# Performance work log

Measured on AMD Instinct MI355X. Metric: run time of the kernel, lower is better.

Reference implementation:

```python
import jax, jax.numpy as jnp
import numpy as np
from jax import lax

EPS = 1e-5

def _conv(x, w, b, stride, pad):
    y = lax.conv_general_dilated(x, w, (stride, stride), ((pad, pad), (pad, pad)),
                                 dimension_numbers=('NCHW', 'OIHW', 'NCHW'))
    return y + b[None, :, None, None]

def _deconv(x, w, b):
    # torch ConvTranspose2d(k=4, s=2, p=1): weight (Cin, Cout, 4, 4)
    w2 = jnp.flip(w, (2, 3)).transpose(1, 0, 2, 3)  # OIHW for forward conv
    y = lax.conv_general_dilated(x, w2, (1, 1), ((2, 2), (2, 2)),
                                 lhs_dilation=(2, 2),
                                 dimension_numbers=('NCHW', 'OIHW', 'NCHW'))
    return y + b[None, :, None, None]

def _bn(x, g, b):
    m = jnp.mean(x, axis=(0, 2, 3), keepdims=True)
    v = jnp.mean((x - m) ** 2, axis=(0, 2, 3), keepdims=True)
    return g[None, :, None, None] * (x - m) * lax.rsqrt(v + EPS) + b[None, :, None, None]

def setup_inputs() -> dict:
    key = jax.random.key(0)
    ks = jax.random.split(key, 16)
    f32 = jnp.float32
    def w(k, shape):
        return (jax.random.normal(k, shape, f32) * 0.05)
    inp = {
        'x': jax.random.uniform(ks[0], (32, 1, 512, 512), f32),
        'w1': w(ks[1], (16, 1, 4, 4)),  'b1': jnp.zeros((16,), f32), 'g1': jnp.ones((16,), f32), 'be1': jnp.zeros((16,), f32),
        'w2': w(ks[2], (16, 16, 4, 4)), 'b2': jnp.zeros((16,), f32), 'g2': jnp.ones((16,), f32), 'be2': jnp.zeros((16,), f32),
        'w3': w(ks[3], (4, 16, 4, 4)),  'b3': jnp.zeros((4,), f32),  'g3': jnp.ones((4,), f32),  'be3': jnp.zeros((4,), f32),
        'wpre': w(ks[4], (2, 4, 1, 1)), 'bpre': jnp.zeros((2,), f32),
        'codebook': w(ks[5], (256, 2)),
        'wpost': w(ks[6], (4, 2, 1, 1)), 'bpost': jnp.zeros((4,), f32),
        'wd1': w(ks[7], (4, 16, 4, 4)),  'bd1': jnp.zeros((16,), f32), 'g4': jnp.ones((16,), f32), 'be4': jnp.zeros((16,), f32),
        'wd2': w(ks[8], (16, 16, 4, 4)), 'bd2': jnp.zeros((16,), f32), 'g5': jnp.ones((16,), f32), 'be5': jnp.zeros((16,), f32),
        'wd3': w(ks[9], (16, 1, 4, 4)),  'bd3': jnp.zeros((1,), f32),
    }
    return inp

def _forward(x, w1, b1, g1, be1, w2, b2, g2, be2, w3, b3, g3, be3,
             wpre, bpre, codebook, wpost, bpost,
             wd1, bd1, g4, be4, wd2, bd2, g5, be5, wd3, bd3):
    # encoder: three stride-2 convs with BN + ReLU
    h = jax.nn.relu(_bn(_conv(x, w1, b1, 2, 1), g1, be1))
    h = jax.nn.relu(_bn(_conv(h, w2, b2, 2, 1), g2, be2))
    h = jax.nn.relu(_bn(_conv(h, w3, b3, 2, 1), g3, be3))
    q = _conv(h, wpre, bpre, 1, 0)          # [B, 2, H/8, W/8]
    B, C, Hq, Wq = q.shape
    qf = q.transpose(0, 2, 3, 1).reshape(B * Hq * Wq, C)   # [N, 2]
    # squared Euclidean distances to codebook (argmin equals cdist argmin)
    d2 = (jnp.sum(qf * qf, -1, keepdims=True)
          - 2.0 * qf @ codebook.T
          + jnp.sum(codebook * codebook, -1)[None, :])     # [N, 256]
    idx = jnp.argmin(d2, axis=-1)
    quant = codebook[idx]                                   # gather [N, 2]
    commitment_loss = jnp.mean((lax.stop_gradient(quant) - qf) ** 2)
    codebook_loss = jnp.mean((quant - lax.stop_gradient(qf)) ** 2)
    qout = qf + lax.stop_gradient(quant - qf)               # straight-through
    qout = qout.reshape(B, Hq, Wq, C).transpose(0, 3, 1, 2)
    d = _conv(qout, wpost, bpost, 1, 0)
    d = jax.nn.relu(_bn(_deconv(d, wd1, bd1), g4, be4))
    d = jax.nn.relu(_bn(_deconv(d, wd2, bd2), g5, be5))
    out = jax.nn.sigmoid(_deconv(d, wd3, bd3))
    recon = jnp.mean((x - out) ** 2)
    total = 1.0 * recon + codebook_loss + 0.2 * commitment_loss
    return out, total

def reference(x, w1, b1, g1, be1, w2, b2, g2, be2, w3, b3, g3, be3,
              wpre, bpre, codebook, wpost, bpost,
              wd1, bd1, g4, be4, wd2, bd2, g5, be5, wd3, bd3):
    return _forward(x, w1, b1, g1, be1, w2, b2, g2, be2, w3, b3, g3, be3,
                    wpre, bpre, codebook, wpost, bpost,
                    wd1, bd1, g4, be4, wd2, bd2, g5, be5, wd3, bd3)
```

## Files before the change

### kernel.cpp

```cpp
#include <hip/hip_runtime.h>
#include <hip/hip_bf16.h>
#include <math.h>

using bf16 = __hip_bfloat16;

__device__ __forceinline__ float b2f(bf16 v) { return __bfloat162float(v); }
__device__ __forceinline__ float ldv(const void* p, size_t i, int m) {
  return m ? b2f(((const bf16*)p)[i]) : ((const float*)p)[i];
}

struct D2 { double s, s2; };

__device__ __forceinline__ void block_stats1(float v, D2* slot) {
  float v2 = v * v;
#pragma unroll
  for (int o = 32; o; o >>= 1) { v += __shfl_down(v, o, 64); v2 += __shfl_down(v2, o, 64); }
  __shared__ float a1[4], a2[4];
  int lane = threadIdx.x & 63, w = threadIdx.x >> 6;
  if (lane == 0) { a1[w] = v; a2[w] = v2; }
  __syncthreads();
  if (threadIdx.x == 0) {
    slot->s  = (double)a1[0] + a1[1] + a1[2] + a1[3];
    slot->s2 = (double)a2[0] + a2[1] + a2[2] + a2[3];
  }
}

__device__ __forceinline__ void block_stats1d(double v, double v2, D2* slot) {
#pragma unroll
  for (int o = 32; o; o >>= 1) { v += __shfl_down(v, o, 64); v2 += __shfl_down(v2, o, 64); }
  __shared__ double q1[4], q2[4];
  int lane = threadIdx.x & 63, w = threadIdx.x >> 6;
  if (lane == 0) { q1[w] = v; q2[w] = v2; }
  __syncthreads();
  if (threadIdx.x == 0) { slot->s = q1[0] + q1[1] + q1[2] + q1[3]; slot->s2 = q2[0] + q2[1] + q2[2] + q2[3]; }
}

__device__ __forceinline__ void block_sum1(float v, double* slot) {
#pragma unroll
  for (int o = 32; o; o >>= 1) v += __shfl_down(v, o, 64);
  __shared__ float a1[4];
  int lane = threadIdx.x & 63, w = threadIdx.x >> 6;
  if (lane == 0) a1[w] = v;
  __syncthreads();
  if (threadIdx.x == 0) *slot = (double)a1[0] + a1[1] + a1[2] + a1[3];
}

__device__ __forceinline__ void block_stats16(const float* vs, const float* vq, D2* base, int NB, int bx) {
  __shared__ float s1[64], s2[64];
  int lane = threadIdx.x & 63, w = threadIdx.x >> 6;
#pragma unroll
  for (int co = 0; co < 16; co++) {
    float v = vs[co], v2 = vq[co];
#pragma unroll
    for (int o = 32; o; o >>= 1) { v += __shfl_down(v, o, 64); v2 += __shfl_down(v2, o, 64); }
    if (lane == 0) { s1[co * 4 + w] = v; s2[co * 4 + w] = v2; }
  }
  __syncthreads();
  if (threadIdx.x < 16) {
    int co = threadIdx.x;
    base[co * NB + bx].s  = (double)s1[co * 4] + s1[co * 4 + 1] + s1[co * 4 + 2] + s1[co * 4 + 3];
    base[co * NB + bx].s2 = (double)s2[co * 4] + s2[co * 4 + 1] + s2[co * 4 + 2] + s2[co * 4 + 3];
  }
}

__global__ void init_k(const unsigned* __restrict__ xw, int* flag) {
  unsigned lo = xw[threadIdx.x] & 0xFFFFu;
  int inr = (lo >= 0x3000u && lo < 0x4000u) ? 1 : 0;
  unsigned long long b = __ballot(inr);
  __shared__ int cnt[4];
  if ((threadIdx.x & 63) == 0) cnt[threadIdx.x >> 6] = __popcll(b);
  __syncthreads();
  if (threadIdx.x == 0) *flag = (cnt[0] + cnt[1] + cnt[2] + cnt[3] >= 128) ? 1 : 0;
}

__global__ void prep_k(const void* w1, const void* b1, const void* w2, const void* b2,
                       const void* w3, const void* b3, const void* wpre, const void* bpre,
                       const void* cbk, const void* wpost, const void* bpost,
                       const void* wd1, const void* bd1, const void* wd2, const void* bd2,
                       const void* wd3, const void* bd3,
                       const void* g1, const void* be1, const void* g2, const void* be2,
                       const void* g3, const void* be3, const void* g4, const void* be4,
                       const void* g5, const void* be5,
                       float* __restrict__ PF, double* __restrict__ PD, const int* modep) {
  int m = *modep, t = threadIdx.x;
  for (int i = t; i < 256; i += 256) PF[i] = ldv(w1, i, m);
  if (t < 16) PF[256 + t] = ldv(b1, t, m);
  for (int i = t; i < 4096; i += 256) {
    int cig = i >> 10, tap = (i >> 6) & 15, c4 = (i >> 4) & 3, co = i & 15;
    PF[272 + i] = ldv(w2, co * 256 + (cig * 4 + c4) * 16 + tap, m);
  }
  if (t < 16) PF[4368 + t] = ldv(b2, t, m);
  for (int i = t; i < 1024; i += 256) {
    int co = i >> 6, ci = (i >> 4) & 3, tap = i & 15;
    PF[4384 + i] = ldv(wd1, ci * 256 + co * 16 + tap, m);
  }
  if (t < 16) PF[5408 + t] = ldv(bd1, t, m);
  for (int i = t; i < 4096; i += 256) {
    int co = i >> 8, ci = (i >> 4) & 15, tap = i & 15;
    PF[5424 + i] = ldv(wd2, ci * 256 + co * 16 + tap, m);
  }
  for (int i = t; i < 4096; i += 256) {
    int ci = i >> 8, tap = (i >> 4) & 15, co = i & 15;
    PF[10272 + i] = ldv(wd2, ci * 256 + co * 16 + tap, m);
  }
  if (t < 16) PF[9520 + t] = ldv(bd2, t, m);
  for (int i = t; i < 256; i += 256) PF[9536 + i] = ldv(wd3, i, m);
  {
    int tap = t >> 4, ci = t & 15;
    PF[10016 + t] = ldv(wd3, ci * 16 + tap, m);
  }
  if (t == 0) PF[9792] = ldv(bd3, 0, m);
  if (t < 16) {
    PF[9856 + t] = ldv(g1, t, m);  PF[9872 + t] = ldv(be1, t, m);
    PF[9888 + t] = ldv(g2, t, m);  PF[9904 + t] = ldv(be2, t, m);
    PF[9952 + t] = ldv(g4, t, m);  PF[9968 + t] = ldv(be4, t, m);
    PF[9984 + t] = ldv(g5, t, m);  PF[10000 + t] = ldv(be5, t, m);
  }
  if (t < 4) { PF[9920 + t] = ldv(g3, t, m); PF[9936 + t] = ldv(be3, t, m); }
  for (int i = t; i < 1024; i += 256) PD[i] = ldv(w3, i, m);
  if (t < 4) PD[1024 + t] = ldv(b3, t, m);
  if (t < 8) PD[1028 + t] = ldv(wpre, t, m);
  if (t < 2) PD[1036 + t] = ldv(bpre, t, m);
  for (int i = t; i < 512; i += 256) PD[1040 + i] = ldv(cbk, i, m);
  if (t < 8) PD[1552 + t] = ldv(wpost, t, m);
  if (t < 4) PD[1560 + t] = ldv(bpost, t, m);
}

__global__ __launch_bounds__(256) void bn_reduce_k(const D2* __restrict__ part, int NB,
                                                   double* __restrict__ stD, float* __restrict__ stF,
                                                   const float* __restrict__ gb, double invN) {
  int c = blockIdx.x;
  double s = 0, s2 = 0;
  for (int i = threadIdx.x; i < NB; i += 256) { D2 p = part[c * NB + i]; s += p.s; s2 += p.s2; }
#pragma unroll
  for (int o = 32; o; o >>= 1) { s += __shfl_down(s, o, 64); s2 += __shfl_down(s2, o, 64); }
  __shared__ double l1[4], l2[4];
  int lane = threadIdx.x & 63, w = threadIdx.x >> 6;
  if (lane == 0) { l1[w] = s; l2[w] = s2; }
  __syncthreads();
  if (threadIdx.x == 0) {
    double S = l1[0] + l1[1] + l1[2] + l1[3], Q = l2[0] + l2[1] + l2[2] + l2[3];
    double mu = S * invN, var = Q * invN - mu * mu;
    if (var < 0) var = 0;
    double sc = (double)gb[c] / sqrt(var + 1e-5);
    double sh = (double)gb[16 + c] - mu * sc;
    stD[c] = sc; stD[16 + c] = sh;
    stF[c] = (float)sc; stF[16 + c] = (float)sh;
  }
}

__global__ __launch_bounds__(256) void conv1_t(const void* __restrict__ x, const float* __restrict__ PF,
                                               float* __restrict__ y, D2* __restrict__ part,
                                               const int* modep) {
  const int m = *modep;
  __shared__ float sx[10 * 130];
  int t = threadIdx.x;
  int bx = blockIdx.x;
  int b = bx >> 8, r = bx & 255, tY = r >> 2, tX = r & 3;
  int iy0 = 8 * tY - 1, ix0 = 128 * tX - 1;
  size_t xb = (size_t)b * 262144;
  for (int i = t; i < 1300; i += 256) {
    int ry = i / 130, rx = i - ry * 130;
    int gy = iy0 + ry, gx = ix0 + rx;
    float v = 0.f;
    if ((unsigned)gy < 512u && (unsigned)gx < 512u) v = ldv(x, xb + (size_t)gy * 512 + gx, m);
    sx[i] = v;
  }
  __syncthreads();
  int tyy = t >> 6, txx = t & 63;
  int oy = tY * 4 + tyy, ox = tX * 64 + txx;
  float acc[16];
#pragma unroll
  for (int co = 0; co < 16; co++) acc[co] = PF[256 + co];
  int ly = 2 * tyy, lx = 2 * txx;
#pragma unroll
  for (int ky = 0; ky < 4; ky++) {
#pragma unroll
    for (int kx = 0; kx < 4; kx++) {
      float v = sx[(ly + ky) * 130 + lx + kx];
#pragma unroll
      for (int co = 0; co < 16; co++) acc[co] = fmaf(v, PF[co * 16 + ky * 4 + kx], acc[co]);
    }
  }
  size_t pix = (size_t)b * 65536 + (size_t)(oy * 256 + ox);
  *(float4*)(y + 0 * 8388608 + pix * 4) = make_float4(acc[0],  acc[1],  acc[2],  acc[3]);
  *(float4*)(y + 1 * 8388608 + pix * 4) = make_float4(acc[4],  acc[5],  acc[6],  acc[7]);
  *(float4*)(y + 2 * 8388608 + pix * 4) = make_float4(acc[8],  acc[9],  acc[10], acc[11]);
  *(float4*)(y + 3 * 8388608 + pix * 4) = make_float4(acc[12], acc[13], acc[14], acc[15]);
  float vq_[16];
#pragma unroll
  for (int co = 0; co < 16; co++) vq_[co] = acc[co] * acc[co];
  block_stats16(acc, vq_, part, 8192, bx);
}

__device__ __forceinline__ float4 aff_relu4(float4 v, float4 sc, float4 sh) {
  v.x = fmaxf(fmaf(v.x, sc.x, sh.x), 0.f);
  v.y = fmaxf(fmaf(v.y, sc.y, sh.y), 0.f);
  v.z = fmaxf(fmaf(v.z, sc.z, sh.z), 0.f);
  v.w = fmaxf(fmaf(v.w, sc.w, sh.w), 0.f);
  return v;
}

__global__ __launch_bounds__(256, 8) void conv2_t(const float* __restrict__ h1, const float* __restrict__ PF,
                                                  const float* __restrict__ aff, float* __restrict__ h2,
                                                  D2* __restrict__ part) {
  __shared__ float su[4896];
  int t = threadIdx.x, ty = t >> 4, tx = t & 15;
  int bx = blockIdx.x, bb = bx >> 6, r = bx & 63, tY = r >> 3, tX = r & 7;
  int oy = tY * 16 + ty, ox = tX * 16 + tx;
  int iy0 = 32 * tY - 1, ix0 = 32 * tX - 1;
  const float* W2 = PF + 272;
  const float4* A4 = (const float4*)aff;
  float acc[16];
#pragma unroll
  for (int co = 0; co < 16; co++) acc[co] = PF[4368 + co];
#pragma unroll
  for (int g = 0; g < 4; g++) {
    __syncthreads();
    float4 SC = A4[g], SH = A4[4 + g];
    const float* pg = h1 + (size_t)g * 8388608 + (size_t)bb * 262144;
    for (int i = t; i < 1156; i += 256) {
      int riy = i / 34, rix = i - riy * 34;
      int gy = iy0 + riy, gx = ix0 + rix;
      float4 v = make_float4(0.f, 0.f, 0.f, 0.f);
      if ((unsigned)gy < 256u && (unsigned)gx < 256u)
        v = aff_relu4(*(const float4*)(pg + (size_t)(gy * 256 + gx) * 4), SC, SH);
      int s = (rix & 1) * 2448 + riy * 18 + (rix >> 1);
      su[s] = v.x; su[612 + s] = v.y; su[1224 + s] = v.z; su[1836 + s] = v.w;
    }
    __syncthreads();
    const float* wg = W2 + g * 1024;
    int base = 2 * ty * 18 + tx;
#pragma unroll
    for (int ky = 0; ky < 4; ky++) {
#pragma unroll
      for (int kx = 0; kx < 4; kx++) {
        int s = (kx & 1) * 2448 + ky * 18 + (kx >> 1) + base;
        float v0 = su[s], v1 = su[612 + s], v2 = su[1224 + s], v3 = su[1836 + s];
        const float* wt = wg + (ky * 4 + kx) * 64;
#pragma unroll
        for (int co = 0; co < 16; co++) {
          float s0 = fmaf(v0, wt[co], acc[co]);
          float s1 = fmaf(v1, wt[16 + co], s0);
          float s2 = fmaf(v2, wt[32 + co], s1);
          acc[co] = fmaf(v3, wt[48 + co], s2);
        }
      }
    }
  }
  float vq_[16];
#pragma unroll
  for (int co = 0; co < 16; co++) {
    h2[((size_t)(bb * 16 + co) * 128 + oy) * 128 + ox] = acc[co];
    vq_[co] = acc[co] * acc[co];
  }
  block_stats16(acc, vq_, part, 2048, bx);
}

__global__ __launch_bounds__(256) void conv3_k(const float* __restrict__ h2, const double* __restrict__ PD,
                                               const float* __restrict__ aff, double* __restrict__ c3,
                                               D2* __restrict__ part) {
  const int co = blockIdx.y;
  int idx = blockIdx.x * 256 + threadIdx.x;
  int b = idx >> 12, rem = idx & 4095, oy = rem >> 6, ox = rem & 63;
  double acc = PD[1024 + co];
  int iy0 = 2 * oy - 1, ix0 = 2 * ox - 1;
  for (int ci = 0; ci < 16; ci++) {
    const float* ib = h2 + (size_t)(b * 16 + ci) * 16384;
    float sc = aff[ci], sh = aff[16 + ci];
    const double* wr = PD + co * 256 + ci * 16;
#pragma unroll
    for (int ky = 0; ky < 4; ky++) {
      int iy = iy0 + ky;
      if ((unsigned)iy < 128u) {
        const float* row = ib + iy * 128;
#pragma unroll
        for (int kx = 0; kx < 4; kx++) {
          int ix = ix0 + kx;
          if ((unsigned)ix < 128u) {
            float v = fmaxf(fmaf(row[ix], sc, sh), 0.f);
            acc = fma((double)v, wr[ky * 4 + kx], acc);
          }
        }
      }
    }
  }
  c3[(size_t)(b * 4 + co) * 4096 + rem] = acc;
  block_stats1d(acc, acc * acc, part + (co * 512 + blockIdx.x));
}

__global__ __launch_bounds__(256) void vq_k(const double* __restrict__ c3, const double* __restrict__ PD,
                                            const double* __restrict__ stD2, float* __restrict__ d0,
                                            double* __restrict__ vp) {
  __shared__ double cb[512];
  for (int i = threadIdx.x; i < 512; i += 256) cb[i] = PD[1040 + i];
  __syncthreads();
  int pix = blockIdx.x * 256 + threadIdx.x;
  int b = pix >> 12, rem = pix & 4095;
  const double* hb = c3 + (size_t)b * 16384 + rem;
  double q0 = PD[1036], q1 = PD[1037];
#pragma unroll
  for (int ci = 0; ci < 4; ci++) {
    double v = fma(hb[ci * 4096], stD2[ci], stD2[16 + ci]);
    if (v < 0) v = 0;
    q0 = fma(v, PD[1028 + ci], q0);
    q1 = fma(v, PD[1032 + ci], q1);
  }
  int best = 0;
  double bd = 1e300;
  for (int k = 0; k < 256; k++) {
    double dx = q0 - cb[2 * k], dy = q1 - cb[2 * k + 1];
    double d = dx * dx + dy * dy;
    if (d < bd) { bd = d; best = k; }
  }
  double c0 = cb[2 * best], c1 = cb[2 * best + 1];
  double e0 = q0 - c0, e1 = q1 - c1;
  float* ob = d0 + (size_t)b * 16384 + rem;
#pragma unroll
  for (int c = 0; c < 4; c++)
    ob[c * 4096] = (float)(PD[1560 + c] + PD[1552 + 2 * c] * c0 + PD[1552 + 2 * c + 1] * c1);
  double v = e0 * e0 + e1 * e1;
#pragma unroll
  for (int o = 32; o; o >>= 1) v += __shfl_down(v, o, 64);
  __shared__ double l1[4];
  int lane = threadIdx.x & 63, w = threadIdx.x >> 6;
  if (lane == 0) l1[w] = v;
  __syncthreads();
  if (threadIdx.x == 0) vp[blockIdx.x] = l1[0] + l1[1] + l1[2] + l1[3];
}

__global__ __launch_bounds__(256) void deconv1_k(const float* __restrict__ d0, const float* __restrict__ PF,
                                                 float* __restrict__ d1, D2* __restrict__ part) {
  const int co = blockIdx.y;
  __shared__ float wl[64];
  if (threadIdx.x < 64) wl[threadIdx.x] = PF[4384 + co * 64 + threadIdx.x];
  __syncthreads();
  int idx = blockIdx.x * 256 + threadIdx.x;
  int b = idx >> 14, rem = idx & 16383, oy = rem >> 7, ox = rem & 127;
  float acc = PF[5408 + co];
  int ry = (oy + 1) & 1, rx = (ox + 1) & 1;
#pragma unroll
  for (int ci = 0; ci < 4; ci++) {
    const float* ib = d0 + (size_t)(b * 4 + ci) * 4096;
    const float* wr = wl + ci * 16;
#pragma unroll
    for (int t2y = 0; t2y < 2; t2y++) {
      int ky = ry + 2 * t2y, iy = (oy + 1 - ky) >> 1;
      if ((unsigned)iy < 64u) {
#pragma unroll
        for (int t2x = 0; t2x < 2; t2x++) {
          int kx = rx + 2 * t2x, ix = (ox + 1 - kx) >> 1;
          if ((unsigned)ix < 64u) acc = fmaf(ib[iy * 64 + ix], wr[ky * 4 + kx], acc);
        }
      }
    }
  }
  d1[(size_t)(b * 16 + co) * 16384 + rem] = acc;
  block_stats1(acc, part + (co * 2048 + blockIdx.x));
}

__global__ __launch_bounds__(256) void deconv2_t(const float* __restrict__ d1, const float* __restrict__ PF,
                                                 const float* __restrict__ aff, float* __restrict__ d2,
                                                 D2* __restrict__ part) {
  __shared__ float su[16 * 324];
  int t = threadIdx.x, py = t >> 4, px = t & 15;
  int bx = blockIdx.x, bb = bx >> 6, r = bx & 63, tY = r >> 3, tX = r & 7;
  int iy0 = 16 * tY - 1, ix0 = 16 * tX - 1;
  for (int i = t; i < 5184; i += 256) {
    int ci = i / 324, rr = i - ci * 324;
    int riy = rr / 18, rix = rr - riy * 18;
    int gy = iy0 + riy, gx = ix0 + rix;
    float v = 0.f;
    if ((unsigned)gy < 128u && (unsigned)gx < 128u)
      v = fmaxf(fmaf(d1[(size_t)(bb * 16 + ci) * 16384 + gy * 128 + gx], aff[ci], aff[16 + ci]), 0.f);
    su[i] = v;
  }
  __syncthreads();
  const float* WT = PF + 10272;
  float vs[16], vq[16];
#pragma unroll
  for (int co = 0; co < 16; co++) { vs[co] = 0.f; vq[co] = 0.f; }
#pragma unroll
  for (int a = 0; a < 2; a++) {
#pragma unroll
    for (int bc = 0; bc < 2; bc++) {
      float acc[16];
#pragma unroll
      for (int co = 0; co < 16; co++) acc[co] = PF[9520 + co];
      int base = (py + a) * 18 + (px + bc);
      for (int ci = 0; ci < 16; ci++) {
        const float* sb = su + ci * 324 + base;
        float v00 = sb[0], v01 = sb[1], v10 = sb[18], v11 = sb[19];
        const float* wci = WT + ci * 256;
        const float* w00p = wci + (((3 - a) * 4 + (3 - bc)) << 4);
        const float* w01p = wci + (((3 - a) * 4 + (1 - bc)) << 4);
        const float* w10p = wci + (((1 - a) * 4 + (3 - bc)) << 4);
        const float* w11p = wci + (((1 - a) * 4 + (1 - bc)) << 4);
#pragma unroll
        for (int co = 0; co < 16; co++) {
          float s0 = fmaf(v00, w00p[co], acc[co]);
          float s1 = fmaf(v01, w01p[co], s0);
          float s2 = fmaf(v10, w10p[co], s1);
          acc[co] = fmaf(v11, w11p[co], s2);
        }
      }
      int oy = 32 * tY + 2 * py + a, ox = 32 * tX + 2 * px + bc;
      float4* dst = (float4*)(d2 + ((size_t)bb * 65536 + (size_t)oy * 256 + ox) * 16);
      dst[0] = make_float4(acc[0],  acc[1],  acc[2],  acc[3]);
      dst[1] = make_float4(acc[4],  acc[5],  acc[6],  acc[7]);
      dst[2] = make_float4(acc[8],  acc[9],  acc[10], acc[11]);
      dst[3] = make_float4(acc[12], acc[13], acc[14], acc[15]);
#pragma unroll
      for (int co = 0; co < 16; co++) {
        vs[co] += acc[co];
        vq[co] = fmaf(acc[co], acc[co], vq[co]);
      }
    }
  }
  block_stats16(vs, vq, part, 2048, bx);
}

__device__ __forceinline__ int swz(int p, int g) {
  int s = p * 4 + (g ^ (p & 3));
  return s ^ (((p >> 2) & 1) << 2);
}

__device__ __forceinline__ float4 aff_relu(float4 v, float4 sc, float4 sh) {
  v.x = fmaxf(fmaf(v.x, sc.x, sh.x), 0.f);
  v.y = fmaxf(fmaf(v.y, sc.y, sh.y), 0.f);
  v.z = fmaxf(fmaf(v.z, sc.z, sh.z), 0.f);
  v.w = fmaxf(fmaf(v.w, sc.w, sh.w), 0.f);
  return v;
}

__device__ __forceinline__ void dot4(float& a, float4 v, float4 w) {
  a = fmaf(v.x, w.x, a); a = fmaf(v.y, w.y, a);
  a = fmaf(v.z, w.z, a); a = fmaf(v.w, w.w, a);
}

__global__ __launch_bounds__(256, 4) void deconv3_t(const float* __restrict__ d2, const float* __restrict__ PF,
                                                    const float* __restrict__ aff, const void* __restrict__ x,
                                                    void* __restrict__ outp, double* __restrict__ rp,
                                                    const int* __restrict__ modep) {
  const int m = *modep;
  __shared__ float4 sd4[1296];
  int t = threadIdx.x;
  int bx = blockIdx.x;
  int b = bx >> 8, r = bx & 255, tY = r >> 4, tX = r & 15;
  int iy0 = 16 * tY - 1, ix0 = 16 * tX - 1;
  const float4* A4 = (const float4*)aff;
  float4 SC0 = A4[0], SC1 = A4[1], SC2 = A4[2], SC3 = A4[3];
  float4 SH0 = A4[4], SH1 = A4[5], SH2 = A4[6], SH3 = A4[7];
  const float* db = d2 + (size_t)b * 1048576;
  for (int p = t; p < 324; p += 256) {
    int riy = p / 18, rix = p - riy * 18;
    int gy = iy0 + riy, gx = ix0 + rix;
    float4 v0, v1, v2, v3;
    if ((unsigned)gy < 256u && (unsigned)gx < 256u) {
      const float4* s = (const float4*)(db + ((size_t)gy * 256 + gx) * 16);
      v0 = aff_relu(s[0], SC0, SH0);
      v1 = aff_relu(s[1], SC1, SH1);
      v2 = aff_relu(s[2], SC2, SH2);
      v3 = aff_relu(s[3], SC3, SH3);
    } else {
      v0 = v1 = v2 = v3 = make_float4(0.f, 0.f, 0.f, 0.f);
    }
    sd4[swz(p, 0)] = v0; sd4[swz(p, 1)] = v1; sd4[swz(p, 2)] = v2; sd4[swz(p, 3)] = v3;
  }
  __syncthreads();

  int lx = t & 15, ly = t >> 4;
  float bias = PF[9792];
  float a00 = bias, a01 = bias, a10 = bias, a11 = bias;
  const float* WT = PF + 10016;
  int p00 = ly * 18 + lx;
#define TAPW(ky, kx) (*(const float4*)(WT + ((ky) * 4 + (kx)) * 16 + (g << 2)))
#pragma unroll
  for (int g = 0; g < 4; g++) {
    float4 w33 = TAPW(3, 3), w31 = TAPW(3, 1), w32 = TAPW(3, 2), w30 = TAPW(3, 0);
    float4 w13 = TAPW(1, 3), w11 = TAPW(1, 1), w12 = TAPW(1, 2), w10 = TAPW(1, 0);
    float4 w23 = TAPW(2, 3), w21 = TAPW(2, 1), w22 = TAPW(2, 2), w20 = TAPW(2, 0);
    float4 w03 = TAPW(0, 3), w01 = TAPW(0, 1), w02 = TAPW(0, 2), w00 = TAPW(0, 0);
    float4 v;
    v = sd4[swz(p00, g)];      dot4(a00, v, w33);
    v = sd4[swz(p00 + 1, g)];  dot4(a00, v, w31); dot4(a01, v, w32);
    v = sd4[swz(p00 + 2, g)];  dot4(a01, v, w30);
    v = sd4[swz(p00 + 18, g)]; dot4(a00, v, w13); dot4(a10, v, w23);
    v = sd4[swz(p00 + 19, g)]; dot4(a00, v, w11); dot4(a01, v, w12); dot4(a10, v, w21); dot4(a11, v, w22);
    v = sd4[swz(p00 + 20, g)]; dot4(a01, v, w10); dot4(a11, v, w20);
    v = sd4[swz(p00 + 36, g)]; dot4(a10, v, w03);
    v = sd4[swz(p00 + 37, g)]; dot4(a10, v, w01); dot4(a11, v, w02);
    v = sd4[swz(p00 + 38, g)]; dot4(a11, v, w00);
  }
#undef TAPW

  int oy = 32 * tY + 2 * ly, ox = 32 * tX + 2 * lx;
  size_t ob = (size_t)b * 262144 + (size_t)oy * 512 + ox;
  float o0 = 1.f / (1.f + expf(-a00));
  float o1 = 1.f / (1.f + expf(-a01));
  float o2 = 1.f / (1.f + expf(-a10));
  float o3 = 1.f / (1.f + expf(-a11));
  if (m) {
    bf16* op = (bf16*)outp;
    op[ob] = __float2bfloat16(o0);       op[ob + 1] = __float2bfloat16(o1);
    op[ob + 512] = __float2bfloat16(o2); op[ob + 513] = __float2bfloat16(o3);
  } else {
    float* op = (float*)outp;
    op[ob] = o0;       op[ob + 1] = o1;
    op[ob + 512] = o2; op[ob + 513] = o3;
  }
  float d0_ = ldv(x, ob, m) - o0;
  float d1_ = ldv(x, ob + 1, m) - o1;
  float d2_ = ldv(x, ob + 512, m) - o2;
  float d3_ = ldv(x, ob + 513, m) - o3;
  float ds = fmaf(d0_, d0_, fmaf(d1_, d1_, fmaf(d2_, d2_, d3_ * d3_)));
  block_sum1(ds, rp + bx);
}

__global__ __launch_bounds__(256) void finalize_k(const double* __restrict__ vp, const double* __restrict__ rp,
                                                  void* outp, const int* modep) {
  double s = 0, rr = 0;
  for (int i = threadIdx.x; i < 512; i += 256) s += vp[i];
  for (int i = threadIdx.x; i < 8192; i += 256) rr += rp[i];
#pragma unroll
  for (int o = 32; o; o >>= 1) { s += __shfl_down(s, o, 64); rr += __shfl_down(rr, o, 64); }
  __shared__ double l1[4], l2[4];
  int lane = threadIdx.x & 63, w = threadIdx.x >> 6;
  if (lane == 0) { l1[w] = s; l2[w] = rr; }
  __syncthreads();
  if (threadIdx.x == 0) {
    double S = l1[0] + l1[1] + l1[2] + l1[3], R = l2[0] + l2[1] + l2[2] + l2[3];
    double total = R * (1.0 / 8388608.0) + 1.2 * (S * (1.0 / 262144.0));
    if (*modep) ((bf16*)outp)[8388608] = __float2bfloat16((float)total);
    else        ((float*)outp)[8388608] = (float)total;
  }
}

extern "C" void kernel_launch(void* const* d_in, const int* in_sizes, int n_in,
                              void* d_out, int out_size, void* d_ws, size_t ws_size,
                              hipStream_t stream) {
  const void* x    = d_in[0];
  const void* w1   = d_in[1];  const void* b1  = d_in[2];
  const void* g1   = d_in[3];  const void* be1 = d_in[4];
  const void* w2   = d_in[5];  const void* b2  = d_in[6];
  const void* g2   = d_in[7];  const void* be2 = d_in[8];
  const void* w3   = d_in[9];  const void* b3  = d_in[10];
  const void* g3   = d_in[11]; const void* be3 = d_in[12];
  const void* wpre = d_in[13]; const void* bpre= d_in[14];
  const void* cbk  = d_in[15];
  const void* wpost= d_in[16]; const void* bpost= d_in[17];
  const void* wd1  = d_in[18]; const void* bd1 = d_in[19];
  const void* g4   = d_in[20]; const void* be4 = d_in[21];
  const void* wd2  = d_in[22]; const void* bd2 = d_in[23];
  const void* g5   = d_in[24]; const void* be5 = d_in[25];
  const void* wd3  = d_in[26]; const void* bd3 = d_in[27];

  char* ws = (char*)d_ws;
  int*    MODE = (int*)ws;
  float*  STF  = (float*)(ws + 1024);
  double* STD  = (double*)(ws + 4096);
  float*  PF   = (float*)(ws + 8192);
  double* PD   = (double*)(ws + 73728);
  D2*     P1   = (D2*)(ws + 131072);
  D2*     P2   = (D2*)(ws + 2228224);
  D2*     P3   = (D2*)(ws + 2752512);
  D2*     P4   = (D2*)(ws + 2785280);
  D2*     P5   = (D2*)(ws + 3309568);
  double* VP   = (double*)(ws + 3833856);
  double* RP   = (double*)(ws + 3837952);
  char* HB = ws + 6291456;
  float*  H1  = (float*)HB;
  float*  H2  = (float*)(HB + 134217728);
  double* C3  = (double*)HB;
  float*  D0  = (float*)(HB + 165675008);
  float*  D1  = (float*)HB;
  float*  D2T = (float*)(HB + 33554432);

  init_k<<<1, 256, 0, stream>>>((const unsigned*)x, MODE);
  prep_k<<<1, 256, 0, stream>>>(w1, b1, w2, b2, w3, b3, wpre, bpre, cbk, wpost, bpost,
                                wd1, bd1, wd2, bd2, wd3, bd3,
                                g1, be1, g2, be2, g3, be3, g4, be4, g5, be5, PF, PD, MODE);

  conv1_t<<<8192, 256, 0, stream>>>(x, PF, H1, P1, MODE);
  bn_reduce_k<<<16, 256, 0, stream>>>(P1, 8192, STD + 0, STF + 0, PF + 9856, 1.0 / 2097152.0);

  conv2_t<<<2048, 256, 0, stream>>>(H1, PF, STF + 0, H2, P2);
  bn_reduce_k<<<16, 256, 0, stream>>>(P2, 2048, STD + 32, STF + 32, PF + 9888, 1.0 / 524288.0);

  conv3_k<<<dim3(512, 4), 256, 0, stream>>>(H2, PD, STF + 32, C3, P3);
  bn_reduce_k<<<4, 256, 0, stream>>>(P3, 512, STD + 64, STF + 64, PF + 9920, 1.0 / 131072.0);

  vq_k<<<512, 256, 0, stream>>>(C3, PD, STD + 64, D0, VP);

  deconv1_k<<<dim3(2048, 16), 256, 0, stream>>>(D0, PF, D1, P4);
  bn_reduce_k<<<16, 256, 0, stream>>>(P4, 2048, STD + 96, STF + 96, PF + 9952, 1.0 / 524288.0);

  deconv2_t<<<2048, 256, 0, stream>>>(D1, PF, STF + 96, D2T, P5);
  bn_reduce_k<<<16, 256, 0, stream>>>(P5, 2048, STD + 128, STF + 128, PF + 9984, 1.0 / 2097152.0);

  deconv3_t<<<8192, 256, 0, stream>>>(D2T, PF, STF + 128, x, d_out, RP, MODE);
  finalize_k<<<1, 256, 0, stream>>>(VP, RP, d_out, MODE);
}
```

Before: 596.1 us.

## Compute all output channels per thread in conv3 and deconv1, store d1 channel-grouped

conv3 now computes all four output channels per thread instead of one channel per block row, so each input load is reused four times. deconv1 is restructured by output phase: each thread computes all 16 output channels for one sub-pixel position from pre-transposed weights, and writes d1 in a float4 channel-group-interleaved layout. deconv2's staging load is changed to read that layout with float4 loads and applies the affine+relu per group. The aim is to remove redundant input reads and the 16x grid replication, at the cost of more registers per thread and a layout change that deconv2 must match.

```diff
diff --git a/kernel.cpp b/kernel.cpp
--- a/kernel.cpp
+++ b/kernel.cpp
@@ -25,14 +25,22 @@
   }
 }
 
-__device__ __forceinline__ void block_stats1d(double v, double v2, D2* slot) {
-#pragma unroll
-  for (int o = 32; o; o >>= 1) { v += __shfl_down(v, o, 64); v2 += __shfl_down(v2, o, 64); }
-  __shared__ double q1[4], q2[4];
+__device__ __forceinline__ void block_stats1d4(const double* v, const double* vq, D2* base, int NB, int bx) {
+  __shared__ double q1[16], q2[16];
   int lane = threadIdx.x & 63, w = threadIdx.x >> 6;
-  if (lane == 0) { q1[w] = v; q2[w] = v2; }
-  __syncthreads();
-  if (threadIdx.x == 0) { slot->s = q1[0] + q1[1] + q1[2] + q1[3]; slot->s2 = q2[0] + q2[1] + q2[2] + q2[3]; }
+#pragma unroll
+  for (int k = 0; k < 4; k++) {
+    double s = v[k], s2 = vq[k];
+#pragma unroll
+    for (int o = 32; o; o >>= 1) { s += __shfl_down(s, o, 64); s2 += __shfl_down(s2, o, 64); }
+    if (lane == 0) { q1[k * 4 + w] = s; q2[k * 4 + w] = s2; }
+  }
+  __syncthreads();
+  if (threadIdx.x < 4) {
+    int k = threadIdx.x;
+    base[k * NB + bx].s  = q1[k * 4] + q1[k * 4 + 1] + q1[k * 4 + 2] + q1[k * 4 + 3];
+    base[k * NB + bx].s2 = q2[k * 4] + q2[k * 4 + 1] + q2[k * 4 + 2] + q2[k * 4 + 3];
+  }
 }
 
 __device__ __forceinline__ void block_sum1(float v, double* slot) {
@@ -93,6 +101,10 @@
   for (int i = t; i < 1024; i += 256) {
     int co = i >> 6, ci = (i >> 4) & 3, tap = i & 15;
     PF[4384 + i] = ldv(wd1, ci * 256 + co * 16 + tap, m);
+  }
+  for (int i = t; i < 1024; i += 256) {
+    int ci = i >> 8, tap = (i >> 4) & 15, co = i & 15;
+    PF[14368 + i] = ldv(wd1, ci * 256 + co * 16 + tap, m);
   }
   if (t < 16) PF[5408 + t] = ldv(bd1, t, m);
   for (int i = t; i < 4096; i += 256) {
@@ -260,15 +272,14 @@
 __global__ __launch_bounds__(256) void conv3_k(const float* __restrict__ h2, const double* __restrict__ PD,
                                                const float* __restrict__ aff, double* __restrict__ c3,
                                                D2* __restrict__ part) {
-  const int co = blockIdx.y;
   int idx = blockIdx.x * 256 + threadIdx.x;
   int b = idx >> 12, rem = idx & 4095, oy = rem >> 6, ox = rem & 63;
-  double acc = PD[1024 + co];
+  double a0 = PD[1024], a1 = PD[1025], a2 = PD[1026], a3 = PD[1027];
   int iy0 = 2 * oy - 1, ix0 = 2 * ox - 1;
   for (int ci = 0; ci < 16; ci++) {
     const float* ib = h2 + (size_t)(b * 16 + ci) * 16384;
     float sc = aff[ci], sh = aff[16 + ci];
-    const double* wr = PD + co * 256 + ci * 16;
+    const double* wr = PD + ci * 16;
 #pragma unroll
     for (int ky = 0; ky < 4; ky++) {
       int iy = iy0 + ky;
@@ -278,15 +289,22 @@
         for (int kx = 0; kx < 4; kx++) {
           int ix = ix0 + kx;
           if ((unsigned)ix < 128u) {
-            float v = fmaxf(fmaf(row[ix], sc, sh), 0.f);
-            acc = fma((double)v, wr[ky * 4 + kx], acc);
+            double v = (double)fmaxf(fmaf(row[ix], sc, sh), 0.f);
+            int tp = ky * 4 + kx;
+            a0 = fma(v, wr[tp], a0);
+            a1 = fma(v, wr[256 + tp], a1);
+            a2 = fma(v, wr[512 + tp], a2);
+            a3 = fma(v, wr[768 + tp], a3);
           }
         }
       }
     }
   }
-  c3[(size_t)(b * 4 + co) * 4096 + rem] = acc;
-  block_stats1d(acc, acc * acc, part + (co * 512 + blockIdx.x));
+  size_t cb = (size_t)b * 16384 + rem;
+  c3[cb] = a0; c3[cb + 4096] = a1; c3[cb + 8192] = a2; c3[cb + 12288] = a3;
+  double vs[4] = {a0, a1, a2, a3};
+  double vq[4] = {a0 * a0, a1 * a1, a2 * a2, a3 * a3};
+  block_stats1d4(vs, vq, part, 512, blockIdx.x);
 }
 
 __global__ __launch_bounds__(256) void vq_k(const double* __restrict__ c3, const double* __restrict__ PD,
@@ -331,32 +349,46 @@
 
 __global__ __launch_bounds__(256) void deconv1_k(const float* __restrict__ d0, const float* __restrict__ PF,
                                                  float* __restrict__ d1, D2* __restrict__ part) {
-  const int co = blockIdx.y;
-  __shared__ float wl[64];
-  if (threadIdx.x < 64) wl[threadIdx.x] = PF[4384 + co * 64 + threadIdx.x];
-  __syncthreads();
+  int phase = blockIdx.y, a = phase >> 1, bc = phase & 1;
   int idx = blockIdx.x * 256 + threadIdx.x;
-  int b = idx >> 14, rem = idx & 16383, oy = rem >> 7, ox = rem & 127;
-  float acc = PF[5408 + co];
-  int ry = (oy + 1) & 1, rx = (ox + 1) & 1;
-#pragma unroll
-  for (int ci = 0; ci < 4; ci++) {
-    const float* ib = d0 + (size_t)(b * 4 + ci) * 4096;
-    const float* wr = wl + ci * 16;
-#pragma unroll
-    for (int t2y = 0; t2y < 2; t2y++) {
-      int ky = ry + 2 * t2y, iy = (oy + 1 - ky) >> 1;
-      if ((unsigned)iy < 64u) {
-#pragma unroll
-        for (int t2x = 0; t2x < 2; t2x++) {
-          int kx = rx + 2 * t2x, ix = (ox + 1 - kx) >> 1;
-          if ((unsigned)ix < 64u) acc = fmaf(ib[iy * 64 + ix], wr[ky * 4 + kx], acc);
+  int b = idx >> 12, rem = idx & 4095, qy = rem >> 6, qx = rem & 63;
+  const float* WT = PF + 14368;
+  float acc[16];
+#pragma unroll
+  for (int co = 0; co < 16; co++) acc[co] = PF[5408 + co];
+  const float* hb = d0 + (size_t)b * 16384;
+#pragma unroll
+  for (int t2y = 0; t2y < 2; t2y++) {
+    int iy = qy + a - t2y;
+    if ((unsigned)iy < 64u) {
+      int kyo = (1 - a + 2 * t2y) * 4;
+#pragma unroll
+      for (int t2x = 0; t2x < 2; t2x++) {
+        int ix = qx + bc - t2x;
+        if ((unsigned)ix < 64u) {
+          int tap = kyo + (1 - bc + 2 * t2x);
+          int off = iy * 64 + ix;
+#pragma unroll
+          for (int ci = 0; ci < 4; ci++) {
+            float v = hb[ci * 4096 + off];
+            const float* wt = WT + ci * 256 + tap * 16;
+#pragma unroll
+            for (int co = 0; co < 16; co++) acc[co] = fmaf(v, wt[co], acc[co]);
+          }
         }
       }
     }
   }
-  d1[(size_t)(b * 16 + co) * 16384 + rem] = acc;
-  block_stats1(acc, part + (co * 2048 + blockIdx.x));
+  int oy = 2 * qy + a, ox = 2 * qx + bc;
+  size_t pix = (size_t)b * 16384 + (size_t)(oy * 128 + ox);
+  *(float4*)(d1 + 0 * 2097152 + pix * 4) = make_float4(acc[0],  acc[1],  acc[2],  acc[3]);
+  *(float4*)(d1 + 1 * 2097152 + pix * 4) = make_float4(acc[4],  acc[5],  acc[6],  acc[7]);
+  *(float4*)(d1 + 2 * 2097152 + pix * 4) = make_float4(acc[8],  acc[9],  acc[10], acc[11]);
+  *(float4*)(d1 + 3 * 2097152 + pix * 4) = make_float4(acc[12], acc[13], acc[14], acc[15]);
+  float vq_[16];
+#pragma unroll
+  for (int co = 0; co < 16; co++) vq_[co] = acc[co] * acc[co];
+  block_stats16(acc, vq_, part, 2048, blockIdx.y * 512 + blockIdx.x);
 }
 
 __global__ __launch_bounds__(256) void deconv2_t(const float* __restrict__ d1, const float* __restrict__ PF,
@@ -366,14 +398,18 @@
   int t = threadIdx.x, py = t >> 4, px = t & 15;
   int bx = blockIdx.x, bb = bx >> 6, r = bx & 63, tY = r >> 3, tX = r & 7;
   int iy0 = 16 * tY - 1, ix0 = 16 * tX - 1;
-  for (int i = t; i < 5184; i += 256) {
-    int ci = i / 324, rr = i - ci * 324;
+  const float4* A4 = (const float4*)aff;
+  for (int i = t; i < 1296; i += 256) {
+    int g = i / 324, rr = i - g * 324;
     int riy = rr / 18, rix = rr - riy * 18;
     int gy = iy0 + riy, gx = ix0 + rix;
-    float v = 0.f;
+    float4 v = make_float4(0.f, 0.f, 0.f, 0.f);
     if ((unsigned)gy < 128u && (unsigned)gx < 128u)
-      v = fmaxf(fmaf(d1[(size_t)(bb * 16 + ci) * 16384 + gy * 128 + gx], aff[ci], aff[16 + ci]), 0.f);
-    su[i] = v;
+      v = aff_relu4(*(const float4*)(d1 + (size_t)g * 2097152 +
+                                     ((size_t)bb * 16384 + (size_t)(gy * 128 + gx)) * 4),
+                    A4[g], A4[4 + g]);
+    int s0 = g * 1296 + rr;
+    su[s0] = v.x; su[s0 + 324] = v.y; su[s0 + 648] = v.z; su[s0 + 972] = v.w;
   }
   __syncthreads();
   const float* WT = PF + 10272;
@@ -587,12 +623,12 @@
   conv2_t<<<2048, 256, 0, stream>>>(H1, PF, STF + 0, H2, P2);
   bn_reduce_k<<<16, 256, 0, stream>>>(P2, 2048, STD + 32, STF + 32, PF + 9888, 1.0 / 524288.0);
 
-  conv3_k<<<dim3(512, 4), 256, 0, stream>>>(H2, PD, STF + 32, C3, P3);
+  conv3_k<<<512, 256, 0, stream>>>(H2, PD, STF + 32, C3, P3);
   bn_reduce_k<<<4, 256, 0, stream>>>(P3, 512, STD + 64, STF + 64, PF + 9920, 1.0 / 131072.0);
 
   vq_k<<<512, 256, 0, stream>>>(C3, PD, STD + 64, D0, VP);
 
-  deconv1_k<<<dim3(2048, 16), 256, 0, stream>>>(D0, PF, D1, P4);
+  deconv1_k<<<dim3(512, 4), 256, 0, stream>>>(D0, PF, D1, P4);
   bn_reduce_k<<<16, 256, 0, stream>>>(P4, 2048, STD + 96, STF + 96, PF + 9952, 1.0 / 524288.0);
 
   deconv2_t<<<2048, 256, 0, stream>>>(D1, PF, STF + 96, D2T, P5);
```

New measurement: 548.1 us. 1.09x faster.
